# Performance work log

Hardware: AMD Instinct MI355X
Metric: run time of the kernel (lower is better)

The kernel has to match this reference:

```python
import jax, jax.numpy as jnp
import numpy as np
import math

# BDH config (defaults from BDHConfig)
D = 256        # n_embd
NH = 4         # n_head
MULT = 128     # mlp_internal_dim_multiplier
N = MULT * D // NH   # 8192 latent dim per head
NLAYER = 6
VOCAB = 256
B, T = 1, 1024
THETA = 2.0 ** 16
TWO_PI = 2.0 * math.pi


def _freqs(n):
    # get_freqs: quantize exponent to even integers
    t = jnp.arange(n, dtype=jnp.float32)
    q = jnp.floor(t / 2.0) * 2.0
    return 1.0 / (THETA ** (q / n)) / TWO_PI  # [N]


def _ln(x, eps=1e-5):
    # LayerNorm without affine params (elementwise_affine=False)
    m = jnp.mean(x, axis=-1, keepdims=True)
    v = jnp.mean((x - m) ** 2, axis=-1, keepdims=True)
    return (x - m) / jnp.sqrt(v + eps)


def _rope(phases, v):
    # phases: [T,N] broadcastable to v [...,T,N]
    ph = (phases % 1.0) * TWO_PI
    cos, sin = jnp.cos(ph), jnp.sin(ph)
    # rotate adjacent pairs: (-v_odd, v_even) interleaved
    vrot = jnp.stack((-v[..., 1::2], v[..., ::2]), axis=-1).reshape(v.shape)
    return v * cos + vrot * sin


def setup_inputs() -> dict:
    key = jax.random.key(0)
    ks = jax.random.split(key, 6)
    std = 0.02
    return {
        "idx": jax.random.randint(ks[0], (B, T), 0, VOCAB),
        "embed_w": jax.random.normal(ks[1], (VOCAB, D), jnp.float32) * std,
        "encoder": jax.random.normal(ks[2], (NH, D, N), jnp.float32) * std,
        "encoder_v": jax.random.normal(ks[3], (NH, D, N), jnp.float32) * std,
        "decoder": jax.random.normal(ks[4], (NH * N, D), jnp.float32) * std,
        "lm_head": jax.random.normal(ks[5], (D, VOCAB), jnp.float32) * std,
    }


def reference(idx, embed_w, encoder, encoder_v, decoder, lm_head):
    freqs = _freqs(N)                                             # [N]
    phases = jnp.arange(T, dtype=jnp.float32)[:, None] * freqs    # [T,N]
    mask = jnp.tril(jnp.ones((T, T), jnp.float32), k=-1)          # strict causal
    dec = decoder.reshape(NH, N, D)

    x = _ln(embed_w[idx])                                         # [B,T,D]
    for _ in range(NLAYER):
        x_sp = jax.nn.relu(jnp.einsum('btd,hdn->bhtn', x, encoder))   # [B,nh,T,N]
        qr = _rope(phases, x_sp)                                       # [B,nh,T,N]
        scores = jnp.einsum('bhtn,bhsn->bhts', qr, qr) * mask          # [B,nh,T,T]
        ykv = _ln(jnp.einsum('bhts,bsd->bhtd', scores, x))             # [B,nh,T,D]
        y_sp = jax.nn.relu(jnp.einsum('bhtd,hdn->bhtn', ykv, encoder_v))
        xy = x_sp * y_sp                                               # [B,nh,T,N]
        ymlp = jnp.einsum('bhtn,hnd->btd', xy, dec)                    # [B,T,D]
        x = _ln(x + _ln(ymlp))
    return x @ lm_head                                                 # [B,T,VOCAB]
```

## Files before the change

kernel.cpp:

```cpp
#include <hip/hip_runtime.h>
#include <hip/hip_bf16.h>
#include <math.h>

#define T_ 1024
#define D_ 256
#define N_ 8192
#define NH_ 4
#define NLAYER_ 6
#define VOCAB_ 256
#define TWO_PI_F 6.283185307179586f

typedef __attribute__((ext_vector_type(8))) short short8;
typedef __attribute__((ext_vector_type(4))) float floatx4;
typedef unsigned short ushort_t;

__device__ __forceinline__ void cp16(const void* g, void* l) {
    __builtin_amdgcn_global_load_lds((const __attribute__((address_space(1))) unsigned int*)g,
                                     (__attribute__((address_space(3))) unsigned int*)l,
                                     16, 0, 0);
}

__device__ __forceinline__ float bf2f_raw(unsigned short u) {
    union { unsigned int i; float f; } x;
    x.i = ((unsigned int)u) << 16;
    return x.f;
}
__device__ __forceinline__ unsigned int f2bf_u(float f) {
    union { float f; unsigned int u; } x; x.f = f;
    return (x.u + 0x7fffu + ((x.u >> 16) & 1u)) >> 16;
}

__device__ __forceinline__ float block_sum(float v, float* red) {
    int tid = threadIdx.x;
    red[tid] = v;
    __syncthreads();
    #pragma unroll
    for (int s = 128; s > 0; s >>= 1) {
        if (tid < s) red[tid] += red[tid + s];
        __syncthreads();
    }
    float r = red[0];
    __syncthreads();
    return r;
}


__global__ void k_embed_ln(const int* __restrict__ idx, const float* __restrict__ ew,
                           float* __restrict__ x, __hip_bfloat16* __restrict__ x_bf) {
    __shared__ float red[256];
    int t = blockIdx.x, d = threadIdx.x;
    float v = ew[idx[t] * D_ + d];
    float mean = block_sum(v, red) * (1.0f / D_);
    float c = v - mean;
    float var = block_sum(c * c, red) * (1.0f / D_);
    float o = c * rsqrtf(var + 1e-5f);
    x[t * D_ + d] = o;
    x_bf[t * D_ + d] = __float2bfloat16(o);
}

__global__ void k_ln_rows(const float* __restrict__ yp, __hip_bfloat16* __restrict__ outb) {
    __shared__ float red[256];
    int r = blockIdx.x, d = threadIdx.x;
    const size_t S = (size_t)NH_ * T_ * D_;
    float v = yp[(size_t)r * D_ + d] + yp[S + (size_t)r * D_ + d];
    float mean = block_sum(v, red) * (1.0f / D_);
    float c = v - mean;
    float var = block_sum(c * c, red) * (1.0f / D_);
    outb[(size_t)r * D_ + d] = __float2bfloat16(c * rsqrtf(var + 1e-5f));
}

__global__ void k_x_update(float* __restrict__ x, const float* __restrict__ ypart,
                           __hip_bfloat16* __restrict__ x_bf) {
    __shared__ float red[256];
    int t = blockIdx.x, d = threadIdx.x;
    float v = 0.0f;
    #pragma unroll
    for (int i = 0; i < 32; i++) v += ypart[(size_t)i * T_ * D_ + t * D_ + d];
    float m1 = block_sum(v, red) * (1.0f / D_);
    float c1 = v - m1;
    float v1 = block_sum(c1 * c1, red) * (1.0f / D_);
    float u = c1 * rsqrtf(v1 + 1e-5f);
    float w = x[t * D_ + d] + u;
    float m2 = block_sum(w, red) * (1.0f / D_);
    float c2 = w - m2;
    float v2 = block_sum(c2 * c2, red) * (1.0f / D_);
    float o = c2 * rsqrtf(v2 + 1e-5f);
    x[t * D_ + d] = o;
    x_bf[t * D_ + d] = __float2bfloat16(o);
}

__global__ __launch_bounds__(256) void k_tcvt(const float* __restrict__ in,
                                              __hip_bfloat16* __restrict__ out,
                                              int R, int C) {
    int h = blockIdx.z;
    int r0 = blockIdx.y * 32, c0 = blockIdx.x * 32;
    __shared__ float tile[32][33];
    int tx = threadIdx.x & 31, ty = threadIdx.x >> 5;
    const float* inh = in + (size_t)h * R * C;
    __hip_bfloat16* outh = out + (size_t)h * R * C;
    #pragma unroll
    for (int i = 0; i < 4; i++)
        tile[ty + 8 * i][tx] = inh[(size_t)(r0 + ty + 8 * i) * C + c0 + tx];
    __syncthreads();
    #pragma unroll
    for (int i = 0; i < 4; i++)
        outh[(size_t)(c0 + ty + 8 * i) * R + r0 + tx] = __float2bfloat16(tile[tx][ty + 8 * i]);
}

__global__ void k_rope_tab(unsigned int* __restrict__ tab) {
    int idx = blockIdx.x * 256 + threadIdx.x;
    int t = idx >> 12, j = idx & 4095;
    float freq = exp2f((float)j * (-1.0f / 256.0f)) * 0.15915494309189535f;
    float ph = (float)t * freq;
    ph -= floorf(ph);
    float s, c;
    __sincosf(ph * TWO_PI_F, &s, &c);
    tab[idx] = f2bf_u(c) | (f2bf_u(s) << 16);
}

__device__ __forceinline__ void gemm128(const ushort_t* __restrict__ A,
                                        const ushort_t* __restrict__ B,
                                        int lda, int ldb, int K,
                                        ushort_t* As, ushort_t* Bs,
                                        floatx4 acc[4][4]) {
    const int tid = threadIdx.x;
    const int lane = tid & 63, wid = tid >> 6;
    const int wm = wid >> 1, wn = wid & 1;
    const int quad = lane >> 4, col = lane & 15;
    int srow[4], scol[4];
    #pragma unroll
    for (int i = 0; i < 4; i++) {
        int s = i * 256 + tid;
        srow[i] = s >> 3;
        scol[i] = (s & 7) ^ (srow[i] & 7);
    }
    for (int k0 = 0; k0 < K; k0 += 64) {
        #pragma unroll
        for (int i = 0; i < 4; i++)
            cp16(A + (size_t)srow[i] * lda + k0 + scol[i] * 8,
                 As + (size_t)(i * 256 + wid * 64) * 8);
        #pragma unroll
        for (int i = 0; i < 4; i++)
            cp16(B + (size_t)srow[i] * ldb + k0 + scol[i] * 8,
                 Bs + (size_t)(i * 256 + wid * 64) * 8);
        __syncthreads();
        #pragma unroll
        for (int kk = 0; kk < 2; kk++) {
            short8 af[4], bf[4];
            #pragma unroll
            for (int mi = 0; mi < 4; mi++) {
                int row = wm * 64 + mi * 16 + col;
                int pc = ((kk << 2) + quad) ^ (row & 7);
                af[mi] = *(const short8*)&As[row * 64 + pc * 8];
            }
            #pragma unroll
            for (int ni = 0; ni < 4; ni++) {
                int row = wn * 64 + ni * 16 + col;
                int pc = ((kk << 2) + quad) ^ (row & 7);
                bf[ni] = *(const short8*)&Bs[row * 64 + pc * 8];
            }
            #pragma unroll
            for (int mi = 0; mi < 4; mi++)
                #pragma unroll
                for (int ni = 0; ni < 4; ni++)
                    acc[mi][ni] = __builtin_amdgcn_mfma_f32_16x16x32_bf16(
                        af[mi], bf[ni], acc[mi][ni], 0, 0, 0);
        }
        __syncthreads();
    }
}

#define GEMM_PROLOGUE()                                              \
    __shared__ __align__(16) ushort_t As[128 * 64];                  \
    __shared__ __align__(16) ushort_t Bs[128 * 64];                  \
    floatx4 acc[4][4];                                               \
    _Pragma("unroll") for (int mi = 0; mi < 4; mi++)                 \
        _Pragma("unroll") for (int ni = 0; ni < 4; ni++)             \
            acc[mi][ni] = (floatx4){0.f, 0.f, 0.f, 0.f};             \
    const int lane = threadIdx.x & 63, wid = threadIdx.x >> 6;       \
    const int wm = wid >> 1, wn = wid & 1;                           \
    const int quad = lane >> 4, col = lane & 15;                     \
    const int odd = lane & 1;                                        \
    const int rsel = odd ? 2 : 0, rother = odd ? 0 : 2;

__global__ __launch_bounds__(256) void k_scores_m(const __hip_bfloat16* __restrict__ qr,
                                                  __hip_bfloat16* __restrict__ scp) {
    const int b = blockIdx.x;
    const int ks = b & 3, h = (b >> 2) & 3;
    int i = b >> 4;
    int ti = 0;
    while ((ti + 1) * (ti + 2) / 2 <= i) ti++;
    int si = i - ti * (ti + 1) / 2;
    const int t0 = ti * 128, s0 = si * 128;
    GEMM_PROLOGUE();
    const ushort_t* qh = (const ushort_t*)qr + (size_t)h * T_ * N_ + (size_t)ks * (N_ / 4);
    gemm128(qh + (size_t)t0 * N_, qh + (size_t)s0 * N_, N_, N_, N_ / 4, As, Bs, acc);
    unsigned int* sch = (unsigned int*)(scp + (size_t)ks * NH_ * T_ * T_ + (size_t)h * T_ * T_);
    #pragma unroll
    for (int mi = 0; mi < 4; mi++)
        #pragma unroll
        for (int ni = 0; ni < 4; ni++) {
            const int ss = s0 + wn * 64 + ni * 16 + col;
            const int ss_e = ss & ~1;
            const int rowb = t0 + wm * 64 + mi * 16 + quad * 4;
            #pragma unroll
            for (int rr = 0; rr < 2; rr++) {
                int tt_o = rowb + rother + rr;
                float send = (ss < tt_o) ? acc[mi][ni][rother + rr] : 0.0f;
                float recv = __shfl_xor(send, 1);
                int tt = rowb + rsel + rr;
                float mine = (ss < tt) ? acc[mi][ni][rsel + rr] : 0.0f;
                float lo = odd ? recv : mine, hi = odd ? mine : recv;
                sch[((size_t)tt * T_ + ss_e) >> 1] = f2bf_u(lo) | (f2bf_u(hi) << 16);
            }
        }
}

__global__ void k_sc_cvt(__hip_bfloat16* __restrict__ scp) {
    int i = blockIdx.x;
    int ti = 0;
    while ((ti + 1) * (ti + 2) / 2 <= i) ti++;
    int si = i - ti * (ti + 1) / 2;
    const size_t S2h = (size_t)NH_ * T_ * T_ / 2;
    unsigned int* sp = (unsigned int*)scp;
    size_t b = (size_t)blockIdx.y * T_ * T_ / 2;
    for (int e = threadIdx.x; e < 128 * 64; e += 256) {
        int r = e >> 6, c = e & 63;
        size_t off = b + (((size_t)(ti * 128 + r) * T_ + si * 128) >> 1) + c;
        float lo = 0.f, hi = 0.f;
        #pragma unroll
        for (int s = 0; s < 4; s++) {
            unsigned int w = sp[off + s * S2h];
            lo += bf2f_raw((unsigned short)(w & 0xffff));
            hi += bf2f_raw((unsigned short)(w >> 16));
        }
        sp[off] = f2bf_u(lo) | (f2bf_u(hi) << 16);
    }
}

template <int MODE>
__global__ __launch_bounds__(256) void k_proj_m(const __hip_bfloat16* __restrict__ Abf,
                                                const __hip_bfloat16* __restrict__ Wt,
                                                __hip_bfloat16* __restrict__ out1,
                                                __hip_bfloat16* __restrict__ out2,
                                                const __hip_bfloat16* __restrict__ xsp,
                                                const unsigned int* __restrict__ rtab) {
    const int h = blockIdx.z;
    const int t0 = blockIdx.y * 128, n0 = blockIdx.x * 128;
    GEMM_PROLOGUE();
    const ushort_t* Ah = (const ushort_t*)Abf + (MODE ? (size_t)h * T_ * D_ : (size_t)0)
                         + (size_t)t0 * D_;
    const ushort_t* Bh = (const ushort_t*)Wt + (size_t)h * N_ * D_ + (size_t)n0 * D_;
    gemm128(Ah, Bh, D_, D_, D_, As, Bs, acc);
    unsigned int* o1 = (unsigned int*)out1;
    unsigned int* o2 = (unsigned int*)out2;
    #pragma unroll
    for (int mi = 0; mi < 4; mi++)
        #pragma unroll
        for (int ni = 0; ni < 4; ni++) {
            const int nn_e = (n0 + wn * 64 + ni * 16 + col) & ~1;
            const int rowb = t0 + wm * 64 + mi * 16 + quad * 4;
            #pragma unroll
            for (int rr = 0; rr < 2; rr++) {
                float send = fmaxf(acc[mi][ni][rother + rr], 0.0f);
                float recv = __shfl_xor(send, 1);
                float mine = fmaxf(acc[mi][ni][rsel + rr], 0.0f);
                float ve = odd ? recv : mine, vo = odd ? mine : recv;
                int tt = rowb + rsel + rr;
                size_t o32 = (((size_t)h * T_ + tt) * (size_t)N_ + nn_e) >> 1;
                if (MODE == 0) {
                    o1[o32] = f2bf_u(ve) | (f2bf_u(vo) << 16);
                    unsigned int cs = rtab[(size_t)tt * 4096 + (nn_e >> 1)];
                    float c = bf2f_raw((unsigned short)(cs & 0xffff));
                    float s = bf2f_raw((unsigned short)(cs >> 16));
                    o2[o32] = f2bf_u(ve * c - vo * s) | (f2bf_u(vo * c + ve * s) << 16);
                } else {
                    unsigned int xw = ((const unsigned int*)xsp)[o32];
                    float xe = bf2f_raw((unsigned short)(xw & 0xffff));
                    float xo = bf2f_raw((unsigned short)(xw >> 16));
                    o1[o32] = f2bf_u(ve * xe) | (f2bf_u(vo * xo) << 16);
                }
            }
        }
}

__global__ __launch_bounds__(256) void k_ykv_m(const __hip_bfloat16* __restrict__ sc,
                                               const __hip_bfloat16* __restrict__ xT,
                                               float* __restrict__ ykvp) {
    const int b = blockIdx.x;
    const int h = (b >> 1) & 3, ks = b & 1;
    const int r0 = b >> 3;
    const int d0 = (r0 & 1) * 128, t0 = (r0 >> 1) * 128;
    GEMM_PROLOGUE();
    const int half = (t0 + 128) >> 1;
    const ushort_t* Ah = (const ushort_t*)sc + (size_t)h * T_ * T_ + (size_t)t0 * T_ + ks * half;
    const ushort_t* Bh = (const ushort_t*)xT + (size_t)d0 * T_ + ks * half;
    gemm128(Ah, Bh, T_, T_, half, As, Bs, acc);
    float2* yp = (float2*)(ykvp + (size_t)ks * NH_ * T_ * D_);
    #pragma unroll
    for (int mi = 0; mi < 4; mi++)
        #pragma unroll
        for (int ni = 0; ni < 4; ni++) {
            const int dd_e = (d0 + wn * 64 + ni * 16 + col) & ~1;
            const int rowb = t0 + wm * 64 + mi * 16 + quad * 4;
            #pragma unroll
            for (int rr = 0; rr < 2; rr++) {
                float send = acc[mi][ni][rother + rr];
                float recv = __shfl_xor(send, 1);
                float mine = acc[mi][ni][rsel + rr];
                int tt = rowb + rsel + rr;
                yp[(((size_t)h * T_ + tt) * D_ + dd_e) >> 1] =
                    odd ? make_float2(recv, mine) : make_float2(mine, recv);
            }
        }
}

__global__ __launch_bounds__(256) void k_ymlp_m(const __hip_bfloat16* __restrict__ xy,
                                                const __hip_bfloat16* __restrict__ decT,
                                                float* __restrict__ ypart) {
    const int b = blockIdx.x;
    const int slice = b & 31;
    const int ks = slice >> 2, h = slice & 3;
    const int r0 = b >> 5;
    const int d0 = (r0 & 1) * 128, t0 = (r0 >> 1) * 128;
    GEMM_PROLOGUE();
    const ushort_t* Ah = (const ushort_t*)xy + (size_t)h * T_ * N_ + (size_t)t0 * N_ + ks * 1024;
    const ushort_t* Bh = (const ushort_t*)decT + (size_t)h * D_ * N_ + (size_t)d0 * N_ + ks * 1024;
    gemm128(Ah, Bh, N_, N_, 1024, As, Bs, acc);
    float2* yp = (float2*)(ypart + (size_t)slice * T_ * D_);
    #pragma unroll
    for (int mi = 0; mi < 4; mi++)
        #pragma unroll
        for (int ni = 0; ni < 4; ni++) {
            const int dd_e = (d0 + wn * 64 + ni * 16 + col) & ~1;
            const int rowb = t0 + wm * 64 + mi * 16 + quad * 4;
            #pragma unroll
            for (int rr = 0; rr < 2; rr++) {
                float send = acc[mi][ni][rother + rr];
                float recv = __shfl_xor(send, 1);
                float mine = acc[mi][ni][rsel + rr];
                int tt = rowb + rsel + rr;
                yp[((size_t)tt * D_ + dd_e) >> 1] =
                    odd ? make_float2(recv, mine) : make_float2(mine, recv);
            }
        }
}

__global__ __launch_bounds__(256) void k_lmhead_m(const __hip_bfloat16* __restrict__ x_bf,
                                                  const __hip_bfloat16* __restrict__ lmT,
                                                  float* __restrict__ out) {
    const int v0 = blockIdx.x * 128, t0 = blockIdx.y * 128;
    GEMM_PROLOGUE();
    const ushort_t* Ah = (const ushort_t*)x_bf + (size_t)t0 * D_;
    const ushort_t* Bh = (const ushort_t*)lmT + (size_t)v0 * D_;
    gemm128(Ah, Bh, D_, D_, D_, As, Bs, acc);
    float2* op = (float2*)out;
    #pragma unroll
    for (int mi = 0; mi < 4; mi++)
        #pragma unroll
        for (int ni = 0; ni < 4; ni++) {
            const int vv_e = (v0 + wn * 64 + ni * 16 + col) & ~1;
            const int rowb = t0 + wm * 64 + mi * 16 + quad * 4;
            #pragma unroll
            for (int rr = 0; rr < 2; rr++) {
                float send = acc[mi][ni][rother + rr];
                float recv = __shfl_xor(send, 1);
                float mine = acc[mi][ni][rsel + rr];
                int tt = rowb + rsel + rr;
                op[((size_t)tt * VOCAB_ + vv_e) >> 1] =
                    odd ? make_float2(recv, mine) : make_float2(mine, recv);
            }
        }
}


extern "C" void kernel_launch(void* const* d_in, const int* in_sizes, int n_in,
                              void* d_out, int out_size, void* d_ws, size_t ws_size,
                              hipStream_t stream) {
    const int* idx = (const int*)d_in[0];
    const float* embed_w = (const float*)d_in[1];
    const float* encoder = (const float*)d_in[2];
    const float* encoder_v = (const float*)d_in[3];
    const float* decoder = (const float*)d_in[4];
    const float* lm_head = (const float*)d_in[5];
    float* out = (float*)d_out;

    char* p = (char*)d_ws;
    auto alloc = [&](size_t bytes) {
        char* q = p;
        p += (bytes + 255) & ~(size_t)255;
        return q;
    };
    float* x = (float*)alloc((size_t)T_ * D_ * 4);
    __hip_bfloat16* x_bf = (__hip_bfloat16*)alloc((size_t)T_ * D_ * 2);
    __hip_bfloat16* xT = (__hip_bfloat16*)alloc((size_t)T_ * D_ * 2);
    __hip_bfloat16* ykv_bf = (__hip_bfloat16*)alloc((size_t)NH_ * T_ * D_ * 2);
    __hip_bfloat16* scp = (__hip_bfloat16*)alloc((size_t)4 * NH_ * T_ * T_ * 2);
    __hip_bfloat16* xsp = (__hip_bfloat16*)alloc((size_t)NH_ * T_ * N_ * 2);
    __hip_bfloat16* qr = (__hip_bfloat16*)alloc((size_t)NH_ * T_ * N_ * 2);
    __hip_bfloat16* encT = (__hip_bfloat16*)alloc((size_t)NH_ * N_ * D_ * 2);
    __hip_bfloat16* encvT = (__hip_bfloat16*)alloc((size_t)NH_ * N_ * D_ * 2);
    __hip_bfloat16* decT = (__hip_bfloat16*)alloc((size_t)NH_ * N_ * D_ * 2);
    __hip_bfloat16* lmT = (__hip_bfloat16*)alloc((size_t)VOCAB_ * D_ * 2);
    unsigned int* rtab = (unsigned int*)alloc((size_t)T_ * 4096 * 4);
    float* ypart = (float*)xsp;
    float* ykvp = (float*)(scp + (size_t)NH_ * T_ * T_);

    k_tcvt<<<dim3(N_ / 32, D_ / 32, NH_), 256, 0, stream>>>(encoder, encT, D_, N_);
    k_tcvt<<<dim3(N_ / 32, D_ / 32, NH_), 256, 0, stream>>>(encoder_v, encvT, D_, N_);
    k_tcvt<<<dim3(D_ / 32, N_ / 32, NH_), 256, 0, stream>>>(decoder, decT, N_, D_);
    k_tcvt<<<dim3(VOCAB_ / 32, D_ / 32, 1), 256, 0, stream>>>(lm_head, lmT, D_, VOCAB_);
    k_rope_tab<<<T_ * 4096 / 256, 256, 0, stream>>>(rtab);

    k_embed_ln<<<T_, 256, 0, stream>>>(idx, embed_w, x, x_bf);
    for (int l = 0; l < NLAYER_; l++) {
        k_proj_m<0><<<dim3(N_ / 128, T_ / 128, NH_), 256, 0, stream>>>(x_bf, encT, xsp, qr,
                                                                       nullptr, rtab);
        k_scores_m<<<36 * 16, 256, 0, stream>>>(qr, scp);
        k_sc_cvt<<<dim3(36, NH_), 256, 0, stream>>>(scp);
        k_tcvt<<<dim3(D_ / 32, T_ / 32, 1), 256, 0, stream>>>(x, xT, T_, D_);
        k_ykv_m<<<16 * 8, 256, 0, stream>>>(scp, xT, ykvp);
        k_ln_rows<<<NH_ * T_, 256, 0, stream>>>(ykvp, ykv_bf);
        k_proj_m<1><<<dim3(N_ / 128, T_ / 128, NH_), 256, 0, stream>>>(ykv_bf, encvT, qr ,
                                                                       nullptr, xsp, rtab);
        k_ymlp_m<<<16 * 32, 256, 0, stream>>>(qr, decT, ypart);
        k_x_update<<<T_, 256, 0, stream>>>(x, ypart, x_bf);
    }
    k_lmhead_m<<<dim3(VOCAB_ / 128, T_ / 128), 256, 0, stream>>>(x_bf, lmT, out);
}
```

Before: 1.350 ms.

## Drop x_sp buffer via inverse RoPE, pack causal scores, split K eight ways

The first projection now writes only the rotated qr. The second projection rebuilds x_sp by applying the inverse rotation to qr using an fp32 cos/sin table, which removes one full [NH,T,N] bf16 write and read per layer. Score partials are stored in a packed lower-triangular layout and the K dimension is split 8 ways instead of 4, so the scores kernel launches more blocks and the reduction and ykv kernels touch less memory. The trade-off is rounding error from recovering x_sp out of a bf16-rounded qr, a rope table twice as large, and more partial sums to reduce.

```diff
diff --git a/kernel.cpp b/kernel.cpp
--- a/kernel.cpp
+++ b/kernel.cpp
@@ -9,6 +9,11 @@
 #define NLAYER_ 6
 #define VOCAB_ 256
 #define TWO_PI_F 6.283185307179586f
+
+#define SC_HSTR32 294912u
+#define SC_SSTR32 1179648u
+#define SC_SPLIT_BYTES 4718592u
+#define SC_NSPLIT 8
 
 typedef __attribute__((ext_vector_type(8))) short short8;
 typedef __attribute__((ext_vector_type(4))) float floatx4;
@@ -107,7 +112,7 @@
         outh[(size_t)(c0 + ty + 8 * i) * R + r0 + tx] = __float2bfloat16(tile[tx][ty + 8 * i]);
 }
 
-__global__ void k_rope_tab(unsigned int* __restrict__ tab) {
+__global__ void k_rope_tab(float2* __restrict__ tab) {
     int idx = blockIdx.x * 256 + threadIdx.x;
     int t = idx >> 12, j = idx & 4095;
     float freq = exp2f((float)j * (-1.0f / 256.0f)) * 0.15915494309189535f;
@@ -115,7 +120,7 @@
     ph -= floorf(ph);
     float s, c;
     __sincosf(ph * TWO_PI_F, &s, &c);
-    tab[idx] = f2bf_u(c) | (f2bf_u(s) << 16);
+    tab[idx] = make_float2(c, s);
 }
 
 __device__ __forceinline__ void gemm128(const ushort_t* __restrict__ A,
@@ -186,51 +191,49 @@
 __global__ __launch_bounds__(256) void k_scores_m(const __hip_bfloat16* __restrict__ qr,
                                                   __hip_bfloat16* __restrict__ scp) {
     const int b = blockIdx.x;
-    const int ks = b & 3, h = (b >> 2) & 3;
-    int i = b >> 4;
+    const int slice = b & 31;
+    const int h = slice & 3, ks = slice >> 2;
+    int i = b >> 5;
     int ti = 0;
     while ((ti + 1) * (ti + 2) / 2 <= i) ti++;
     int si = i - ti * (ti + 1) / 2;
     const int t0 = ti * 128, s0 = si * 128;
     GEMM_PROLOGUE();
-    const ushort_t* qh = (const ushort_t*)qr + (size_t)h * T_ * N_ + (size_t)ks * (N_ / 4);
-    gemm128(qh + (size_t)t0 * N_, qh + (size_t)s0 * N_, N_, N_, N_ / 4, As, Bs, acc);
-    unsigned int* sch = (unsigned int*)(scp + (size_t)ks * NH_ * T_ * T_ + (size_t)h * T_ * T_);
+    const ushort_t* qh = (const ushort_t*)qr + (size_t)h * T_ * N_ + (size_t)ks * (N_ / 8);
+    gemm128(qh + (size_t)t0 * N_, qh + (size_t)s0 * N_, N_, N_, N_ / 8, As, Bs, acc);
+    const int W = (ti + 1) * 128;
+    unsigned int* sch = (unsigned int*)scp + (size_t)ks * SC_SSTR32 + (size_t)h * SC_HSTR32
+                        + (size_t)4096 * ti * (ti + 1);
     #pragma unroll
     for (int mi = 0; mi < 4; mi++)
         #pragma unroll
         for (int ni = 0; ni < 4; ni++) {
             const int ss = s0 + wn * 64 + ni * 16 + col;
             const int ss_e = ss & ~1;
-            const int rowb = t0 + wm * 64 + mi * 16 + quad * 4;
+            const int rowb = wm * 64 + mi * 16 + quad * 4;
             #pragma unroll
             for (int rr = 0; rr < 2; rr++) {
                 int tt_o = rowb + rother + rr;
-                float send = (ss < tt_o) ? acc[mi][ni][rother + rr] : 0.0f;
+                float send = (ss < t0 + tt_o) ? acc[mi][ni][rother + rr] : 0.0f;
                 float recv = __shfl_xor(send, 1);
                 int tt = rowb + rsel + rr;
-                float mine = (ss < tt) ? acc[mi][ni][rsel + rr] : 0.0f;
+                float mine = (ss < t0 + tt) ? acc[mi][ni][rsel + rr] : 0.0f;
                 float lo = odd ? recv : mine, hi = odd ? mine : recv;
-                sch[((size_t)tt * T_ + ss_e) >> 1] = f2bf_u(lo) | (f2bf_u(hi) << 16);
+                sch[((size_t)tt * W + ss_e) >> 1] = f2bf_u(lo) | (f2bf_u(hi) << 16);
             }
         }
 }
 
 __global__ void k_sc_cvt(__hip_bfloat16* __restrict__ scp) {
-    int i = blockIdx.x;
-    int ti = 0;
-    while ((ti + 1) * (ti + 2) / 2 <= i) ti++;
-    int si = i - ti * (ti + 1) / 2;
-    const size_t S2h = (size_t)NH_ * T_ * T_ / 2;
     unsigned int* sp = (unsigned int*)scp;
-    size_t b = (size_t)blockIdx.y * T_ * T_ / 2;
-    for (int e = threadIdx.x; e < 128 * 64; e += 256) {
-        int r = e >> 6, c = e & 63;
-        size_t off = b + (((size_t)(ti * 128 + r) * T_ + si * 128) >> 1) + c;
+    unsigned int idx = blockIdx.x * 256 + threadIdx.x;
+    #pragma unroll
+    for (int r = 0; r < 4; r++) {
+        size_t off = (size_t)idx + (size_t)r * SC_HSTR32;
         float lo = 0.f, hi = 0.f;
         #pragma unroll
-        for (int s = 0; s < 4; s++) {
-            unsigned int w = sp[off + s * S2h];
+        for (int s = 0; s < SC_NSPLIT; s++) {
+            unsigned int w = sp[off + (size_t)s * SC_SSTR32];
             lo += bf2f_raw((unsigned short)(w & 0xffff));
             hi += bf2f_raw((unsigned short)(w >> 16));
         }
@@ -242,9 +245,7 @@
 __global__ __launch_bounds__(256) void k_proj_m(const __hip_bfloat16* __restrict__ Abf,
                                                 const __hip_bfloat16* __restrict__ Wt,
                                                 __hip_bfloat16* __restrict__ out1,
-                                                __hip_bfloat16* __restrict__ out2,
-                                                const __hip_bfloat16* __restrict__ xsp,
-                                                const unsigned int* __restrict__ rtab) {
+                                                const float2* __restrict__ rtab) {
     const int h = blockIdx.z;
     const int t0 = blockIdx.y * 128, n0 = blockIdx.x * 128;
     GEMM_PROLOGUE();
@@ -253,7 +254,6 @@
     const ushort_t* Bh = (const ushort_t*)Wt + (size_t)h * N_ * D_ + (size_t)n0 * D_;
     gemm128(Ah, Bh, D_, D_, D_, As, Bs, acc);
     unsigned int* o1 = (unsigned int*)out1;
-    unsigned int* o2 = (unsigned int*)out2;
     #pragma unroll
     for (int mi = 0; mi < 4; mi++)
         #pragma unroll
@@ -268,16 +268,15 @@
                 float ve = odd ? recv : mine, vo = odd ? mine : recv;
                 int tt = rowb + rsel + rr;
                 size_t o32 = (((size_t)h * T_ + tt) * (size_t)N_ + nn_e) >> 1;
+                float2 cs = rtab[(size_t)tt * 4096 + (nn_e >> 1)];
                 if (MODE == 0) {
-                    o1[o32] = f2bf_u(ve) | (f2bf_u(vo) << 16);
-                    unsigned int cs = rtab[(size_t)tt * 4096 + (nn_e >> 1)];
-                    float c = bf2f_raw((unsigned short)(cs & 0xffff));
-                    float s = bf2f_raw((unsigned short)(cs >> 16));
-                    o2[o32] = f2bf_u(ve * c - vo * s) | (f2bf_u(vo * c + ve * s) << 16);
+                    o1[o32] = f2bf_u(ve * cs.x - vo * cs.y) | (f2bf_u(vo * cs.x + ve * cs.y) << 16);
                 } else {
-                    unsigned int xw = ((const unsigned int*)xsp)[o32];
-                    float xe = bf2f_raw((unsigned short)(xw & 0xffff));
-                    float xo = bf2f_raw((unsigned short)(xw >> 16));
+                    unsigned int xw = o1[o32];
+                    float qe = bf2f_raw((unsigned short)(xw & 0xffff));
+                    float qo = bf2f_raw((unsigned short)(xw >> 16));
+                    float xe = qe * cs.x + qo * cs.y;
+                    float xo = qo * cs.x - qe * cs.y;
                     o1[o32] = f2bf_u(ve * xe) | (f2bf_u(vo * xo) << 16);
                 }
             }
@@ -292,10 +291,13 @@
     const int r0 = b >> 3;
     const int d0 = (r0 & 1) * 128, t0 = (r0 >> 1) * 128;
     GEMM_PROLOGUE();
-    const int half = (t0 + 128) >> 1;
-    const ushort_t* Ah = (const ushort_t*)sc + (size_t)h * T_ * T_ + (size_t)t0 * T_ + ks * half;
-    const ushort_t* Bh = (const ushort_t*)xT + (size_t)d0 * T_ + ks * half;
-    gemm128(Ah, Bh, T_, T_, half, As, Bs, acc);
+    const int W = t0 + 128;
+    const int half = W >> 1;
+    const int ti = t0 >> 7;
+    const ushort_t* Ah = (const ushort_t*)sc + (size_t)h * 589824u
+                         + (size_t)8192 * ti * (ti + 1) + (size_t)ks * half;
+    const ushort_t* Bh = (const ushort_t*)xT + (size_t)d0 * T_ + (size_t)ks * half;
+    gemm128(Ah, Bh, W, T_, half, As, Bs, acc);
     float2* yp = (float2*)(ykvp + (size_t)ks * NH_ * T_ * D_);
     #pragma unroll
     for (int mi = 0; mi < 4; mi++)
@@ -395,16 +397,15 @@
     __hip_bfloat16* x_bf = (__hip_bfloat16*)alloc((size_t)T_ * D_ * 2);
     __hip_bfloat16* xT = (__hip_bfloat16*)alloc((size_t)T_ * D_ * 2);
     __hip_bfloat16* ykv_bf = (__hip_bfloat16*)alloc((size_t)NH_ * T_ * D_ * 2);
-    __hip_bfloat16* scp = (__hip_bfloat16*)alloc((size_t)4 * NH_ * T_ * T_ * 2);
-    __hip_bfloat16* xsp = (__hip_bfloat16*)alloc((size_t)NH_ * T_ * N_ * 2);
+    __hip_bfloat16* scp = (__hip_bfloat16*)alloc((size_t)SC_NSPLIT * SC_SPLIT_BYTES);
     __hip_bfloat16* qr = (__hip_bfloat16*)alloc((size_t)NH_ * T_ * N_ * 2);
     __hip_bfloat16* encT = (__hip_bfloat16*)alloc((size_t)NH_ * N_ * D_ * 2);
     __hip_bfloat16* encvT = (__hip_bfloat16*)alloc((size_t)NH_ * N_ * D_ * 2);
     __hip_bfloat16* decT = (__hip_bfloat16*)alloc((size_t)NH_ * N_ * D_ * 2);
     __hip_bfloat16* lmT = (__hip_bfloat16*)alloc((size_t)VOCAB_ * D_ * 2);
-    unsigned int* rtab = (unsigned int*)alloc((size_t)T_ * 4096 * 4);
-    float* ypart = (float*)xsp;
-    float* ykvp = (float*)(scp + (size_t)NH_ * T_ * T_);
+    float2* rtab = (float2*)alloc((size_t)T_ * 4096 * 8);
+    float* ypart = (float*)alloc((size_t)32 * T_ * D_ * 4);
+    float* ykvp = (float*)((char*)scp + SC_SPLIT_BYTES);
 
     k_tcvt<<<dim3(N_ / 32, D_ / 32, NH_), 256, 0, stream>>>(encoder, encT, D_, N_);
     k_tcvt<<<dim3(N_ / 32, D_ / 32, NH_), 256, 0, stream>>>(encoder_v, encvT, D_, N_);
@@ -414,15 +415,14 @@
 
     k_embed_ln<<<T_, 256, 0, stream>>>(idx, embed_w, x, x_bf);
     for (int l = 0; l < NLAYER_; l++) {
-        k_proj_m<0><<<dim3(N_ / 128, T_ / 128, NH_), 256, 0, stream>>>(x_bf, encT, xsp, qr,
-                                                                       nullptr, rtab);
-        k_scores_m<<<36 * 16, 256, 0, stream>>>(qr, scp);
-        k_sc_cvt<<<dim3(36, NH_), 256, 0, stream>>>(scp);
+        k_proj_m<0><<<dim3(N_ / 128, T_ / 128, NH_), 256, 0, stream>>>(x_bf, encT, qr, rtab);
+        k_scores_m<<<36 * 32, 256, 0, stream>>>(qr, scp);
+        k_sc_cvt<<<1152, 256, 0, stream>>>(scp);
         k_tcvt<<<dim3(D_ / 32, T_ / 32, 1), 256, 0, stream>>>(x, xT, T_, D_);
         k_ykv_m<<<16 * 8, 256, 0, stream>>>(scp, xT, ykvp);
         k_ln_rows<<<NH_ * T_, 256, 0, stream>>>(ykvp, ykv_bf);
         k_proj_m<1><<<dim3(N_ / 128, T_ / 128, NH_), 256, 0, stream>>>(ykv_bf, encvT, qr ,
-                                                                       nullptr, xsp, rtab);
+                                                                       rtab);
         k_ymlp_m<<<16 * 32, 256, 0, stream>>>(qr, decT, ypart);
         k_x_update<<<T_, 256, 0, stream>>>(x, ypart, x_bf);
     }
```

Result: slower. 1.604 ms (+18.8%).
